# Optimization experiments

Hardware: AMD Instinct MI355X
Metric: run time of the kernel (lower is better)

Reference implementation:

```python
import jax, jax.numpy as jnp
import numpy as np
from jax import lax

B, C, H, W = 64, 20, 128, 128  # C = 3 target + 16 hidden + 1
LIVING = 3                      # living_channel_dim = num_target_channels
ALIVE_TH = 0.1
FIRE_RATE = 0.5


def setup_inputs() -> dict:
    key = jax.random.key(0)
    ks = jax.random.split(key, 7)
    x = jax.random.normal(ks[0], (B, C, H, W), dtype=jnp.float32)
    goal_encoding = jax.random.normal(ks[1], (B, C, H, W), dtype=jnp.float32)
    rand_uniform = jax.random.uniform(ks[2], (B, 1, H, W), dtype=jnp.float32)
    # depthwise 3x3 perception conv: groups=C, 3 outputs per channel -> OIHW [3C, 1, 3, 3]
    pw = jax.random.normal(ks[3], (3 * C, 1, 3, 3), dtype=jnp.float32) * 0.1
    # update net: 1x1 convs expressed as dense matrices
    w1 = jax.random.normal(ks[4], (128, 3 * C), dtype=jnp.float32) * (1.0 / np.sqrt(3 * C))
    b1 = jnp.zeros((128,), dtype=jnp.float32)  # zero_bias init
    w2 = jax.random.normal(ks[5], (C, 128), dtype=jnp.float32) * (1.0 / np.sqrt(128.0))
    return {"x": x, "goal_encoding": goal_encoding, "rand_uniform": rand_uniform,
            "pw": pw, "w1": w1, "b1": b1, "w2": w2}


def _maxpool3(a):
    # 3x3 max pool, stride 1, SAME padding (torch pads with -inf for max pool)
    return lax.reduce_window(a, -jnp.inf, lax.max, (1, 1, 3, 3), (1, 1, 1, 1), 'SAME')


def _alive(x):
    return _maxpool3(x[:, LIVING:LIVING + 1]) > ALIVE_TH


def reference(x, goal_encoding, rand_uniform, pw, w1, b1, w2):
    pre_life_mask = _alive(x)                                  # [B,1,H,W] bool
    rand_mask = (rand_uniform < FIRE_RATE).astype(x.dtype)     # [B,1,H,W]

    xg = x + goal_encoding * pre_life_mask.astype(x.dtype)
    # depthwise 3x3 perception: feature_group_count = C
    perceive = lax.conv_general_dilated(
        xg, pw, window_strides=(1, 1), padding='SAME',
        feature_group_count=C,
        dimension_numbers=('NCHW', 'OIHW', 'NCHW'))            # [B,3C,H,W]
    # update net: 1x1 conv -> ReLU -> 1x1 conv (no bias)
    h = jax.nn.relu(jnp.einsum('bchw,oc->bohw', perceive, w1) + b1[None, :, None, None])
    out = jnp.einsum('bchw,oc->bohw', h, w2)                   # [B,C,H,W]

    x_new = x + rand_mask * out
    post_life_mask = _alive(x_new)
    life_mask = (pre_life_mask & post_life_mask).astype(x.dtype)
    x_new = jnp.clip(x_new * life_mask, -10.0, 10.0)
    return x_new
```

## Files before the change

kernel.cpp:

```cpp
#include <hip/hip_runtime.h>
#include <hip/hip_bf16.h>


#define BB 64
#define CC 20
#define HH 128
#define WW 128
#define LIVCH 3
#define NPIX (BB*HH*WW)

typedef __attribute__((ext_vector_type(8))) short short8;
typedef __attribute__((ext_vector_type(4))) float f32x4;

#define LDS_FENCE() asm volatile("" ::: "memory")

static __device__ __forceinline__ unsigned short f2bf(float f) {
    __hip_bfloat16 h = __float2bfloat16(f);
    return *reinterpret_cast<unsigned short*>(&h);
}
static __device__ __forceinline__ float bf2f(unsigned short u) {
    union { unsigned int i; float f; } c; c.i = ((unsigned int)u) << 16; return c.f;
}

__global__ __launch_bounds__(256) void nca_prep(const float* __restrict__ w2,
                                                unsigned short* __restrict__ w2f) {
    int gid = blockIdx.x * 256 + threadIdx.x;
    if (gid < 512) {
        int f2 = gid >> 6, lane = gid & 63;
        int ks2 = f2 >> 1, nt2 = f2 & 1;
        int n = nt2 * 16 + (lane & 15), kb = ks2 * 32 + (lane >> 4) * 8;
        short8 o;
        #pragma unroll
        for (int j = 0; j < 8; ++j) {
            float v = (n < CC) ? w2[n * 128 + kb + j] : 0.0f;
            o[j] = (short)f2bf(v);
        }
        *reinterpret_cast<short8*>(w2f + f2 * 512 + lane * 8) = o;
    }
}

__global__ __launch_bounds__(256) void nca_pre_mask(const float* __restrict__ x,
                                                    unsigned char* __restrict__ mpre) {
    int idx = blockIdx.x * 256 + threadIdx.x;
    int w = idx & (WW - 1);
    int h = (idx >> 7) & (HH - 1);
    int b = idx >> 14;
    const float* ch = x + ((size_t)b * CC + LIVCH) * (HH * WW);
    float m = -1e30f;
    #pragma unroll
    for (int dy = -1; dy <= 1; ++dy) {
        int y = h + dy;
        if ((unsigned)y >= HH) continue;
        #pragma unroll
        for (int dx = -1; dx <= 1; ++dx) {
            int xx = w + dx;
            if ((unsigned)xx >= WW) continue;
            m = fmaxf(m, ch[y * WW + xx]);
        }
    }
    mpre[idx] = (m > 0.1f) ? 1 : 0;
}

__global__ __launch_bounds__(512, 2) void nca_main_mfma(
    const float* __restrict__ x, const float* __restrict__ goal,
    const float* __restrict__ rnd, const float* __restrict__ pw,
    const float* __restrict__ w1, const float* __restrict__ b1,
    const unsigned short* __restrict__ w2f, const float* __restrict__ w2,
    const unsigned char* __restrict__ mpre,
    float* __restrict__ xnew, float* __restrict__ ch3out) {

    __shared__ unsigned short w1h[128 * 64];
    __shared__ unsigned short w1l[128 * 64];
    __shared__ float ph_buf[8][16 * 68];

    const int tid  = threadIdx.x;
    const int lane = tid & 63;
    const int wv   = tid >> 6;
    const int blk  = blockIdx.x;
    const int b    = blk >> 5;
    const int y0   = (blk & 31) * 4;

    for (int i = tid; i < 128 * 64; i += 512) {
        int n = i >> 6, k = i & 63;
        float v = (k < 60) ? w1[n * 60 + k] : 0.0f;
        unsigned short hi = f2bf(v);
        int si = (n << 6) + ((((k >> 3) ^ (n & 7)) << 3)) + (k & 7);
        w1h[si] = hi;
        w1l[si] = f2bf(v - bf2f(hi));
    }
    __syncthreads();

    const int y    = y0 + (tid >> 7);
    const int wcol = tid & 127;
    const int dm   = (wcol > 0)   ? 1 : 0;
    const int dp   = (wcol < 127) ? 1 : 0;
    const float fm = (float)dm, fp = (float)dp;

    float p[64];
    #pragma unroll
    for (int i = 0; i < 64; ++i) p[i] = 0.0f;

    #pragma unroll
    for (int dy = -1; dy <= 1; ++dy) {
        int yy = y + dy;
        if (yy >= 0 && yy < HH) {
            const int rb = (b << 14) + (yy << 7) + wcol;
            const float mp_m = (float)mpre[rb - dm];
            const float mp_0 = (float)mpre[rb];
            const float mp_p = (float)mpre[rb + dp];
            #pragma unroll
            for (int c = 0; c < CC; ++c) {
                const int gi  = ((b * CC + c) << 14) + (yy << 7) + wcol;
                const int gim = gi - dm;
                const int gip = gi + dp;
                float vm = __builtin_fmaf(goal[gim], mp_m, x[gim]) * fm;
                float v  = __builtin_fmaf(goal[gi ], mp_0, x[gi ]);
                float vp = __builtin_fmaf(goal[gip], mp_p, x[gip]) * fp;
                #pragma unroll
                for (int kk = 0; kk < 3; ++kk) {
                    const int t = 3 * c + kk;
                    const float* pr = pw + t * 9 + (dy + 1) * 3;
                    p[t] = __builtin_fmaf(pr[0], vm, p[t]);
                    p[t] = __builtin_fmaf(pr[1], v,  p[t]);
                    p[t] = __builtin_fmaf(pr[2], vp, p[t]);
                }
            }
        }
    }

    const int l15 = lane & 15;
    const int l4  = lane >> 4;

    float bias_[8], w2r3[8];
    #pragma unroll
    for (int nt = 0; nt < 8; ++nt) {
        bias_[nt] = b1[nt * 16 + l15];
        w2r3[nt]  = w2[3 * 128 + nt * 16 + l15];
    }
    short8 b2f[2][4];
    #pragma unroll
    for (int nt = 0; nt < 2; ++nt)
        #pragma unroll
        for (int ks = 0; ks < 4; ++ks)
            b2f[nt][ks] = *reinterpret_cast<const short8*>(
                w2f + (ks * 2 + nt) * 512 + lane * 8);

    float*          pbuf = &ph_buf[wv][0];
    unsigned short* hbuf = reinterpret_cast<unsigned short*>(pbuf);

    const int hwbase = ((blk & 31) << 9) + (wv << 6);

    for (int mt = 0; mt < 4; ++mt) {
        LDS_FENCE();
        if (l4 == mt) {
            #pragma unroll
            for (int g = 0; g < 16; ++g) {
                f32x4 t = { p[g*4+0], p[g*4+1], p[g*4+2], p[g*4+3] };
                *reinterpret_cast<f32x4*>(pbuf + l15 * 68 + g * 4) = t;
            }
        }
        LDS_FENCE();

        short8 ah[2], al[2];
        #pragma unroll
        for (int ks = 0; ks < 2; ++ks) {
            f32x4 u0 = *reinterpret_cast<const f32x4*>(pbuf + l15 * 68 + ks * 32 + l4 * 8);
            f32x4 u1 = *reinterpret_cast<const f32x4*>(pbuf + l15 * 68 + ks * 32 + l4 * 8 + 4);
            #pragma unroll
            for (int j = 0; j < 4; ++j) {
                unsigned short h0 = f2bf(u0[j]);
                ah[ks][j]     = (short)h0;
                al[ks][j]     = (short)f2bf(u0[j] - bf2f(h0));
                unsigned short h1 = f2bf(u1[j]);
                ah[ks][4 + j] = (short)h1;
                al[ks][4 + j] = (short)f2bf(u1[j] - bf2f(h1));
            }
        }

        f32x4 C1[8];
        #pragma unroll
        for (int nt = 0; nt < 8; ++nt) {
            f32x4 c = { bias_[nt], bias_[nt], bias_[nt], bias_[nt] };
            #pragma unroll
            for (int ks = 0; ks < 2; ++ks) {
                const int n = nt * 16 + l15;
                const int chunk = (((ks << 2) + l4) ^ (n & 7)) << 3;
                const short8 bh = *reinterpret_cast<const short8*>(w1h + (n << 6) + chunk);
                const short8 bl = *reinterpret_cast<const short8*>(w1l + (n << 6) + chunk);
                c = __builtin_amdgcn_mfma_f32_16x16x32_bf16(ah[ks], bh, c, 0, 0, 0);
                c = __builtin_amdgcn_mfma_f32_16x16x32_bf16(al[ks], bh, c, 0, 0, 0);
                c = __builtin_amdgcn_mfma_f32_16x16x32_bf16(ah[ks], bl, c, 0, 0, 0);
            }
            C1[nt] = c;
        }

        float s[4] = {0.f, 0.f, 0.f, 0.f};
        #pragma unroll
        for (int nt = 0; nt < 8; ++nt) {
            #pragma unroll
            for (int r = 0; r < 4; ++r) {
                float hv = fmaxf(C1[nt][r], 0.0f);
                s[r] = __builtin_fmaf(w2r3[nt], hv, s[r]);
                int hrow = (l4 << 2) + r;
                hbuf[hrow * 136 + ((nt * 16 + l15) ^ ((hrow & 7) << 3))] = f2bf(hv);
            }
        }
        LDS_FENCE();

        f32x4 C2[2];
        C2[0] = (f32x4){0.f, 0.f, 0.f, 0.f};
        C2[1] = (f32x4){0.f, 0.f, 0.f, 0.f};
        #pragma unroll
        for (int ks2 = 0; ks2 < 4; ++ks2) {
            int col0 = (ks2 * 32 + l4 * 8) ^ ((l15 & 7) << 3);
            short8 a2 = *reinterpret_cast<const short8*>(hbuf + l15 * 136 + col0);
            C2[0] = __builtin_amdgcn_mfma_f32_16x16x32_bf16(a2, b2f[0][ks2], C2[0], 0, 0, 0);
            C2[1] = __builtin_amdgcn_mfma_f32_16x16x32_bf16(a2, b2f[1][ks2], C2[1], 0, 0, 0);
        }

        #pragma unroll
        for (int r = 0; r < 4; ++r) {
            s[r] += __shfl_xor(s[r], 1, 64);
            s[r] += __shfl_xor(s[r], 2, 64);
            s[r] += __shfl_xor(s[r], 4, 64);
            s[r] += __shfl_xor(s[r], 8, 64);
        }

        const int hw = hwbase + (mt << 4) + (l4 << 2);
        float4 r4 = *reinterpret_cast<const float4*>(rnd + (b << 14) + hw);
        float rm0 = (r4.x < 0.5f) ? 1.0f : 0.0f;
        float rm1 = (r4.y < 0.5f) ? 1.0f : 0.0f;
        float rm2 = (r4.z < 0.5f) ? 1.0f : 0.0f;
        float rm3 = (r4.w < 0.5f) ? 1.0f : 0.0f;
        #pragma unroll
        for (int nt = 0; nt < 2; ++nt) {
            int o = (nt << 4) + l15;
            if (o < CC) {
                const bool isliv = (nt == 0) && (l15 == LIVCH);
                float u0 = isliv ? s[0] : C2[nt][0];
                float u1 = isliv ? s[1] : C2[nt][1];
                float u2 = isliv ? s[2] : C2[nt][2];
                float u3 = isliv ? s[3] : C2[nt][3];
                int gi = ((b * CC + o) << 14) + hw;
                float4 xo = *reinterpret_cast<const float4*>(x + gi);
                float4 vo;
                vo.x = __builtin_fmaf(rm0, u0, xo.x);
                vo.y = __builtin_fmaf(rm1, u1, xo.y);
                vo.z = __builtin_fmaf(rm2, u2, xo.z);
                vo.w = __builtin_fmaf(rm3, u3, xo.w);
                *reinterpret_cast<float4*>(xnew + gi) = vo;
                if (isliv)
                    *reinterpret_cast<float4*>(ch3out + (b << 14) + hw) = vo;
            }
        }
    }
}

__global__ __launch_bounds__(256) void nca_finalize(const float* __restrict__ ch3,
                                                    const unsigned char* __restrict__ mpre,
                                                    float* __restrict__ xnew) {
    int idx = blockIdx.x * 256 + threadIdx.x;
    int w = idx & (WW - 1);
    int h = (idx >> 7) & (HH - 1);
    int b = idx >> 14;
    const float* plane = ch3 + b * (HH * WW);
    float m = -1e30f;
    #pragma unroll
    for (int dy = -1; dy <= 1; ++dy) {
        int y = h + dy;
        if ((unsigned)y >= HH) continue;
        #pragma unroll
        for (int dx = -1; dx <= 1; ++dx) {
            int xx = w + dx;
            if ((unsigned)xx >= WW) continue;
            m = fmaxf(m, plane[y * WW + xx]);
        }
    }
    bool post = m > 0.1f;
    bool pre = mpre[idx] != 0;
    float life = (pre && post) ? 1.0f : 0.0f;

    size_t base_b = (size_t)b * CC * (HH * WW);
    int pixoff = h * WW + w;
    #pragma unroll
    for (int c = 0; c < CC; ++c) {
        size_t o = base_b + (size_t)c * (HH * WW) + pixoff;
        float v = xnew[o] * life;
        v = fminf(fmaxf(v, -10.0f), 10.0f);
        xnew[o] = v;
    }
}

extern "C" void kernel_launch(void* const* d_in, const int* in_sizes, int n_in,
                              void* d_out, int out_size, void* d_ws, size_t ws_size,
                              hipStream_t stream) {
    const float* x    = (const float*)d_in[0];
    const float* goal = (const float*)d_in[1];
    const float* rnd  = (const float*)d_in[2];
    const float* pw   = (const float*)d_in[3];
    const float* w1   = (const float*)d_in[4];
    const float* b1   = (const float*)d_in[5];
    const float* w2   = (const float*)d_in[6];
    float* out = (float*)d_out;

    unsigned char*  mpre = (unsigned char*)d_ws;
    float*          ch3  = (float*)((char*)d_ws + NPIX);
    unsigned short* w2f  = (unsigned short*)((char*)d_ws + NPIX + (size_t)NPIX * 4);

    dim3 blk(256), grd(NPIX / 256);
    hipLaunchKernelGGL(nca_prep, dim3(2), blk, 0, stream, w2, w2f);
    hipLaunchKernelGGL(nca_pre_mask, grd, blk, 0, stream, x, mpre);
    hipLaunchKernelGGL(nca_main_mfma, dim3(NPIX / 512), dim3(512), 0, stream,
                       x, goal, rnd, pw, w1, b1, w2f, w2, mpre, out, ch3);
    hipLaunchKernelGGL(nca_finalize, grd, blk, 0, stream, ch3, mpre, out);
}
```

Baseline: 262.0 us.

## Stage goal-masked input halo tile in LDS for depthwise perception conv

```diff
diff --git a/kernel.cpp b/kernel.cpp
--- a/kernel.cpp
+++ b/kernel.cpp
@@ -69,9 +69,11 @@
     const unsigned char* __restrict__ mpre,
     float* __restrict__ xnew, float* __restrict__ ch3out) {
 
-    __shared__ unsigned short w1h[128 * 64];
-    __shared__ unsigned short w1l[128 * 64];
-    __shared__ float ph_buf[8][16 * 68];
+    __shared__ __align__(16) char lds_raw[67584];
+    float*          xg   = (float*)lds_raw;
+    unsigned short* w1h  = (unsigned short*)lds_raw;
+    unsigned short* w1l  = (unsigned short*)(lds_raw + 16384);
+    float*          phb  = (float*)(lds_raw + 32768);
 
     const int tid  = threadIdx.x;
     const int lane = tid & 63;
@@ -79,6 +81,50 @@
     const int blk  = blockIdx.x;
     const int b    = blk >> 5;
     const int y0   = (blk & 31) * 4;
+
+    for (int i = tid; i < 20 * 6 * 132; i += 512) {
+        int ch  = i / 792;
+        int rem = i - ch * 792;
+        int r   = rem / 132;
+        int ci  = rem - r * 132;
+        int yy  = y0 - 1 + r;
+        int col = ci - 1;
+        float v = 0.0f;
+        if ((unsigned)yy < HH && (unsigned)col < WW) {
+            int gi = ((b * CC + ch) << 14) + (yy << 7) + col;
+            float m = (float)mpre[(b << 14) + (yy << 7) + col];
+            v = __builtin_fmaf(goal[gi], m, x[gi]);
+        }
+        xg[i] = v;
+    }
+    __syncthreads();
+
+    const int rr   = tid >> 7;
+    const int wcol = tid & 127;
+    const int cbase = rr * 132 + wcol;
+
+    float p[64];
+    #pragma unroll
+    for (int i = 0; i < 64; ++i) p[i] = 0.0f;
+
+    #pragma unroll
+    for (int c = 0; c < CC; ++c) {
+        #pragma unroll
+        for (int dy = 0; dy < 3; ++dy) {
+            const float v0 = xg[c * 792 + dy * 132 + cbase + 0];
+            const float v1 = xg[c * 792 + dy * 132 + cbase + 1];
+            const float v2 = xg[c * 792 + dy * 132 + cbase + 2];
+            #pragma unroll
+            for (int kk = 0; kk < 3; ++kk) {
+                const int t = 3 * c + kk;
+                const float* pr = pw + t * 9 + dy * 3;
+                p[t] = __builtin_fmaf(pr[0], v0, p[t]);
+                p[t] = __builtin_fmaf(pr[1], v1, p[t]);
+                p[t] = __builtin_fmaf(pr[2], v2, p[t]);
+            }
+        }
+    }
+    __syncthreads();
 
     for (int i = tid; i < 128 * 64; i += 512) {
         int n = i >> 6, k = i & 63;
@@ -90,44 +136,6 @@
     }
     __syncthreads();
 
-    const int y    = y0 + (tid >> 7);
-    const int wcol = tid & 127;
-    const int dm   = (wcol > 0)   ? 1 : 0;
-    const int dp   = (wcol < 127) ? 1 : 0;
-    const float fm = (float)dm, fp = (float)dp;
-
-    float p[64];
-    #pragma unroll
-    for (int i = 0; i < 64; ++i) p[i] = 0.0f;
-
-    #pragma unroll
-    for (int dy = -1; dy <= 1; ++dy) {
-        int yy = y + dy;
-        if (yy >= 0 && yy < HH) {
-            const int rb = (b << 14) + (yy << 7) + wcol;
-            const float mp_m = (float)mpre[rb - dm];
-            const float mp_0 = (float)mpre[rb];
-            const float mp_p = (float)mpre[rb + dp];
-            #pragma unroll
-            for (int c = 0; c < CC; ++c) {
-                const int gi  = ((b * CC + c) << 14) + (yy << 7) + wcol;
-                const int gim = gi - dm;
-                const int gip = gi + dp;
-                float vm = __builtin_fmaf(goal[gim], mp_m, x[gim]) * fm;
-                float v  = __builtin_fmaf(goal[gi ], mp_0, x[gi ]);
-                float vp = __builtin_fmaf(goal[gip], mp_p, x[gip]) * fp;
-                #pragma unroll
-                for (int kk = 0; kk < 3; ++kk) {
-                    const int t = 3 * c + kk;
-                    const float* pr = pw + t * 9 + (dy + 1) * 3;
-                    p[t] = __builtin_fmaf(pr[0], vm, p[t]);
-                    p[t] = __builtin_fmaf(pr[1], v,  p[t]);
-                    p[t] = __builtin_fmaf(pr[2], vp, p[t]);
-                }
-            }
-        }
-    }
-
     const int l15 = lane & 15;
     const int l4  = lane >> 4;
 
@@ -145,7 +153,7 @@
             b2f[nt][ks] = *reinterpret_cast<const short8*>(
                 w2f + (ks * 2 + nt) * 512 + lane * 8);
 
-    float*          pbuf = &ph_buf[wv][0];
+    float*          pbuf = phb + wv * 1088;
     unsigned short* hbuf = reinterpret_cast<unsigned short*>(pbuf);
 
     const int hwbase = ((blk & 31) << 9) + (wv << 6);
```

Result: slower. 346.0 us (+32.1%).
